# Optimization experiments

Measured on AMD Instinct MI355X. Metric: run time of the kernel, lower is better.

Reference implementation:

```python
import jax, jax.numpy as jnp
import numpy as np

EPS = 1e-8
NUM = 4


def rot_badmm(x, c1, c2, p0, q0, a0, a1, a2, a3, rho, mask, num=NUM, eps=EPS):
    """Entropic Bregman-ADMM regularized OT solver (badmm-e).
    x:(B,N,D) c1:(B,D,D) c2:(B,N,N) p0:(B,1,D) q0:(B,N,1) mask:(B,N,1)
    a0..a3, rho: (num,). Returns t:(B,N,D)."""
    lse = jax.nn.logsumexp
    log_t = jnp.log(q0 * p0 + eps)          # (B,N,D)
    log_s = log_t
    log_mu = jnp.log(p0)                    # (B,1,D)
    log_eta = jnp.log(q0 + eps)             # (B,N,1)
    log_p0 = jnp.log(p0)
    log_q0 = jnp.log(q0 + eps)
    z = jnp.zeros_like(log_t)
    z1 = jnp.zeros_like(p0)
    z2 = jnp.zeros_like(q0)
    for k in range(num):                    # fixed small unroll (num=4)
        n = min(k, a1.shape[0] - 1)
        tmp2 = jnp.matmul(jnp.matmul(c2, jnp.exp(log_s)), c1)   # (B,N,D)
        y = (x + a0[n] * tmp2 - z) / rho[n] + log_s
        log_t = (log_mu - lse(y, axis=2, keepdims=True)) + y    # row-normalize
        tmp2 = jnp.matmul(jnp.matmul(c2, jnp.exp(log_t)), c1)
        y = (z + a0[n] * tmp2 + rho[n] * log_t) / (a1[n] + rho[n])
        log_s = (log_eta - lse(y, axis=1, keepdims=True)) + y   # col-normalize
        t = jnp.exp(log_t) * mask
        s = jnp.exp(log_s) * mask
        z = z + rho[n] * (t - s)
        y = (rho[n] * log_mu + a2[n] * log_p0 - z1) / (rho[n] + a2[n])
        log_mu = y - lse(y, axis=2, keepdims=True)
        y = (rho[n] * log_eta + a3[n] * log_q0 - z2) / (rho[n] + a3[n])
        log_eta = y - lse(y, axis=1, keepdims=True)
        z1 = z1 + rho[n] * (jnp.exp(log_mu) - jnp.sum(t, axis=2, keepdims=True))
        z2 = z2 + rho[n] * (jnp.exp(log_eta) - jnp.sum(s, axis=1, keepdims=True))
    return jnp.exp(log_t) * mask


def setup_inputs() -> dict:
    key = jax.random.key(0)
    ks = jax.random.split(key, 10)
    B, N, D = 8, 1024, 512
    x = 0.1 * jax.random.normal(ks[0], (B, N, D), dtype=jnp.float32)
    c1 = 0.1 * jax.random.normal(ks[1], (B, D, D), dtype=jnp.float32)
    c2 = 0.1 * jax.random.normal(ks[2], (B, N, N), dtype=jnp.float32)
    p0 = jax.random.uniform(ks[3], (B, 1, D), dtype=jnp.float32) + 0.1
    p0 = p0 / jnp.sum(p0, axis=2, keepdims=True)        # valid marginal over D
    q0 = jax.random.uniform(ks[4], (B, N, 1), dtype=jnp.float32) + 0.1
    q0 = q0 / jnp.sum(q0, axis=1, keepdims=True)        # valid marginal over N
    a0 = jax.random.uniform(ks[5], (NUM,), dtype=jnp.float32) * 0.5 + 0.1
    a1 = jax.random.uniform(ks[6], (NUM,), dtype=jnp.float32) * 0.5 + 0.1
    a2 = jax.random.uniform(ks[7], (NUM,), dtype=jnp.float32) * 0.5 + 0.1
    a3 = jax.random.uniform(ks[8], (NUM,), dtype=jnp.float32) * 0.5 + 0.1
    rho = jax.random.uniform(ks[9], (NUM,), dtype=jnp.float32) * 0.5 + 0.5
    mask = jnp.ones((B, N, 1), dtype=jnp.float32)
    return {"x": x, "c1": c1, "c2": c2, "p0": p0, "q0": q0,
            "a0": a0, "a1": a1, "a2": a2, "a3": a3, "rho": rho,
            "mask": mask, "num": NUM}


def reference(x, c1, c2, p0, q0, a0, a1, a2, a3, rho, mask, num):
    return rot_badmm(x, c1, c2, p0, q0, a0, a1, a2, a3, rho, mask, num=num, eps=EPS)
```

## Files before the change

### kernel.cpp

```cpp
#include <hip/hip_runtime.h>
#include <math.h>

#define B_ 8
#define N_ 1024
#define D_ 512
#define CH 32
#define CHUNK (N_/CH)
#define EPSF 1e-8f

typedef unsigned short u16;
typedef __attribute__((ext_vector_type(8))) short bf16x8;
typedef __attribute__((ext_vector_type(4))) float f32x4;

static __device__ __forceinline__ u16 f2bf(float f){
  unsigned int u = __builtin_bit_cast(unsigned int, f);
  u = (u + 0x7FFFu + ((u >> 16) & 1u)) >> 16;
  return (u16)u;
}

static __device__ __forceinline__ float wredMax(float v){
#pragma unroll
  for (int o=32;o>=1;o>>=1) v = fmaxf(v, __shfl_xor(v,o,64));
  return v;
}
static __device__ __forceinline__ float wredSum(float v){
#pragma unroll
  for (int o=32;o>=1;o>>=1) v += __shfl_xor(v,o,64);
  return v;
}
static __device__ __forceinline__ float blockMax(float v, float* sm){
  v = wredMax(v);
  int w = threadIdx.x>>6, l = threadIdx.x&63;
  if (l==0) sm[w]=v;
  __syncthreads();
  float r = fmaxf(fmaxf(sm[0],sm[1]),fmaxf(sm[2],sm[3]));
  __syncthreads();
  return r;
}
static __device__ __forceinline__ float blockSum(float v, float* sm){
  v = wredSum(v);
  int w = threadIdx.x>>6, l = threadIdx.x&63;
  if (l==0) sm[w]=v;
  __syncthreads();
  float r = (sm[0]+sm[1])+(sm[2]+sm[3]);
  __syncthreads();
  return r;
}

__global__ __launch_bounds__(256)
void init_kernel(float* __restrict__ logS, float* __restrict__ Z,
                 const float* __restrict__ p0, const float* __restrict__ q0)
{
  long i = (long)blockIdx.x*256 + threadIdx.x;
  int d  = (int)(i & (D_-1));
  long bn = i >> 9;
  int b  = (int)(bn >> 10);
  logS[i] = logf(q0[bn]*p0[b*D_+d] + EPSF);
  Z[i] = 0.f;
}

__global__ __launch_bounds__(256)
void margInit_kernel(float* __restrict__ M, float* __restrict__ u,
                     float* __restrict__ Lv, float* __restrict__ p,
                     const float* __restrict__ p0, const float* __restrict__ q0)
{
  int b = blockIdx.x, t = threadIdx.x;
  for (int d = t; d < D_; d += 256){ M[b*D_+d] = logf(p0[b*D_+d]); u[b*D_+d] = 0.f; }
  for (int n = t; n < N_; n += 256){ Lv[b*N_+n] = logf(q0[b*N_+n] + EPSF); p[b*N_+n] = 0.f; }
}

__global__ __launch_bounds__(256)
void initEt_kernel(u16* __restrict__ Et, const float* __restrict__ p0,
                   const float* __restrict__ q0)
{
  long i = (long)blockIdx.x*256 + threadIdx.x;
  int n = (int)(i & (N_-1));
  long bd = i >> 10;
  int d = (int)(bd & (D_-1));
  int b = (int)(bd >> 9);
  Et[i] = f2bf(p0[b*D_+d]*q0[b*N_+n] + EPSF);
}

__global__ __launch_bounds__(256)
void conv_kernel(const float* __restrict__ src, u16* __restrict__ dst)
{
  long i = (long)blockIdx.x*256 + threadIdx.x;
  float4 v = ((const float4*)src)[i];
  ushort4 u;
  u.x=f2bf(v.x); u.y=f2bf(v.y); u.z=f2bf(v.z); u.w=f2bf(v.w);
  ((ushort4*)dst)[i] = u;
}

__global__ __launch_bounds__(256)
void tconv_kernel(const float* __restrict__ src, u16* __restrict__ dst, int R, int Ccols)
{
  __shared__ float tile[64][65];
  const int b = blockIdx.z;
  const long bb = (long)b*R*Ccols;
  const int r0 = blockIdx.x*64, c0 = blockIdx.y*64;
  const int c = threadIdx.x & 63, rr = threadIdx.x >> 6;
#pragma unroll
  for (int i=0;i<16;i++){
    int r = i*4 + rr;
    tile[r][c] = src[bb + (long)(r0+r)*Ccols + c0 + c];
  }
  __syncthreads();
#pragma unroll
  for (int i=0;i<16;i++){
    int r = i*4 + rr;
    dst[bb + (long)(c0+r)*R + r0 + c] = f2bf(tile[c][r]);
  }
}

template<int K, int OUT_BF16>
__global__ __launch_bounds__(256)
void gemm_mfma(const u16* __restrict__ Ab, const u16* __restrict__ Btb,
               void* __restrict__ Cp, long sA, long sB, long sC, int ldc)
{
  __shared__ __attribute__((aligned(16))) u16 As[128*72];
  __shared__ __attribute__((aligned(16))) u16 Bs[64*72];
  const int t = threadIdx.x;
  const int b = blockIdx.z;
  const int row0 = blockIdx.x*128, col0 = blockIdx.y*64;
  const int w = t>>6, l = t&63, lr = l&15, lg = l>>4;
  const int wm = w>>1, wn = w&1;

  f32x4 acc[4][2];
#pragma unroll
  for (int m=0;m<4;m++)
#pragma unroll
    for (int n=0;n<2;n++) acc[m][n] = (f32x4){0.f,0.f,0.f,0.f};

  const u16* Abb = Ab + (long)b*sA + (long)row0*K;
  const u16* Bbb = Btb + (long)b*sB + (long)col0*K;

  bf16x8 qa[4];
  bf16x8 qb[2];

#pragma unroll
  for (int i=0;i<4;i++){ int g=i*256+t; int r=g>>3, j=g&7;
    qa[i] = *(const bf16x8*)(Abb + (long)r*K + j*8); }
#pragma unroll
  for (int i=0;i<2;i++){ int g=i*256+t; int r=g>>3, j=g&7;
    qb[i] = *(const bf16x8*)(Bbb + (long)r*K + j*8); }

  for (int k0 = 0; k0 < K; k0 += 64) {
    __syncthreads();
#pragma unroll
    for (int i=0;i<4;i++){ int g=i*256+t; int r=g>>3, j=g&7;
      *(bf16x8*)&As[r*72 + j*8] = qa[i]; }
#pragma unroll
    for (int i=0;i<2;i++){ int g=i*256+t; int r=g>>3, j=g&7;
      *(bf16x8*)&Bs[r*72 + j*8] = qb[i]; }
    __syncthreads();
    if (k0 + 64 < K) {
      int kn = k0 + 64;
#pragma unroll
      for (int i=0;i<4;i++){ int g=i*256+t; int r=g>>3, j=g&7;
        qa[i] = *(const bf16x8*)(Abb + (long)r*K + kn + j*8); }
#pragma unroll
      for (int i=0;i<2;i++){ int g=i*256+t; int r=g>>3, j=g&7;
        qb[i] = *(const bf16x8*)(Bbb + (long)r*K + kn + j*8); }
    }
#pragma unroll
    for (int kk=0;kk<2;kk++){
      bf16x8 afr[4], bfr[2];
#pragma unroll
      for (int m=0;m<4;m++)
        afr[m] = *(const bf16x8*)&As[(wm*64 + m*16 + lr)*72 + kk*32 + lg*8];
#pragma unroll
      for (int n=0;n<2;n++)
        bfr[n] = *(const bf16x8*)&Bs[(wn*32 + n*16 + lr)*72 + kk*32 + lg*8];
#pragma unroll
      for (int m=0;m<4;m++)
#pragma unroll
        for (int n=0;n<2;n++)
          acc[m][n] = __builtin_amdgcn_mfma_f32_16x16x32_bf16(afr[m], bfr[n], acc[m][n], 0, 0, 0);
    }
  }

  if constexpr (OUT_BF16) {
    u16* C = (u16*)Cp + (long)b*sC;
#pragma unroll
    for (int m=0;m<4;m++)
#pragma unroll
      for (int n=0;n<2;n++){
        int grow = row0 + wm*64 + m*16 + lg*4;
        int gcol = col0 + wn*32 + n*16 + lr;
#pragma unroll
        for (int r4=0;r4<4;r4++)
          C[(long)(grow+r4)*ldc + gcol] = f2bf(acc[m][n][r4]);
      }
  } else {
    float* C = (float*)Cp + (long)b*sC;
#pragma unroll
    for (int m=0;m<4;m++)
#pragma unroll
      for (int n=0;n<2;n++){
        int grow = row0 + wm*64 + m*16 + lg*4;
        int gcol = col0 + wn*32 + n*16 + lr;
#pragma unroll
        for (int r4=0;r4<4;r4++)
          C[(long)(grow+r4)*ldc + gcol] = acc[m][n][r4];
      }
  }
}

__global__ __launch_bounds__(256)
void rowA_kernel(const float* __restrict__ x, const float* __restrict__ P2,
                 const float* __restrict__ Z, const float* __restrict__ logS,
                 const float* __restrict__ M, float* __restrict__ E,
                 const float* __restrict__ a0p, const float* __restrict__ rhop, int it)
{
  __shared__ float sm[4];
  const int bn = blockIdx.x;
  const int b = bn >> 10;
  const long base = (long)bn * D_;
  const float a0 = a0p[it], rho = rhop[it];
  const float inv_rho = 1.f/rho;
  const int d0 = threadIdx.x, d1 = d0 + 256;
  const long i0 = base + d0, i1 = base + d1;
  float y0 = (x[i0] + a0*P2[i0] - Z[i0])*inv_rho + logS[i0];
  float y1 = (x[i1] + a0*P2[i1] - Z[i1])*inv_rho + logS[i1];
  float Mx = blockMax(fmaxf(y0,y1), sm);
  float S = blockSum(expf(y0-Mx)+expf(y1-Mx), sm);
  float lse = Mx + logf(S);
  E[i0] = expf(M[b*D_+d0] - lse + y0);
  E[i1] = expf(M[b*D_+d1] - lse + y1);
}

__global__ __launch_bounds__(256)
void colS1_kernel(float* __restrict__ P2, const float* __restrict__ Z,
                  const float* __restrict__ E,
                  float* __restrict__ pMax, float* __restrict__ pSum,
                  const float* __restrict__ a0p, const float* __restrict__ a1p,
                  const float* __restrict__ rhop, int it)
{
  const int d = blockIdx.x*256 + threadIdx.x;
  const int ch = blockIdx.y, b = blockIdx.z;
  const float a0=a0p[it], rho=rhop[it];
  const float inv = 1.f/(a1p[it]+rho);
  long i = (long)b*N_*D_ + (long)(ch*CHUNK)*D_ + d;
  float m = -INFINITY, s = 0.f;
  for (int n=0;n<CHUNK;n++, i+=D_){
    float lt = logf(E[i] + 1e-37f);
    float yv = (Z[i] + a0*P2[i] + rho*lt)*inv;
    P2[i] = yv;
    float mn = fmaxf(m,yv);
    s = s*expf(m-mn) + expf(yv-mn);
    m = mn;
  }
  long pi = ((long)(b*D_+d))*CH + ch;
  pMax[pi]=m; pSum[pi]=s;
}

__global__ __launch_bounds__(256)
void colS2_kernel(const float* __restrict__ Yp, const float* __restrict__ E,
                  float* __restrict__ logS, float* __restrict__ Z,
                  const float* __restrict__ Lv,
                  const float* __restrict__ pMax, const float* __restrict__ pSum,
                  const float* __restrict__ maskp, u16* __restrict__ Et,
                  const float* __restrict__ rhop, int it)
{
  __shared__ u16 tile[CHUNK][258];
  const int tid = threadIdx.x;
  const int d0 = blockIdx.x*256;
  const int d = d0 + tid;
  const int ch = blockIdx.y, b = blockIdx.z;
  const int n0 = ch*CHUNK;
  const float rho = rhop[it];
  const long bd = (long)(b*D_+d);
  float M = -INFINITY;
#pragma unroll
  for (int c=0;c<CH;c++) M = fmaxf(M, pMax[bd*CH+c]);
  float S = 0.f;
#pragma unroll
  for (int c=0;c<CH;c++) S += pSum[bd*CH+c]*expf(pMax[bd*CH+c]-M);
  const float lseC = M + logf(S);
  long i = (long)b*N_*D_ + (long)n0*D_ + d;
  for (int n=0;n<CHUNK;n++, i+=D_){
    int gn = n0 + n;
    float msk = maskp[b*N_+gn];
    float ls = Lv[b*N_+gn] - lseC + Yp[i];
    logS[i] = ls;
    float es = expf(ls);
    tile[n][tid] = f2bf(es);
    Z[i] += rho*msk*(E[i] - es);
  }
  __syncthreads();
  const long EtBase = ((long)b*D_ + d0)*N_ + n0;
#pragma unroll
  for (int j=0;j<CHUNK;j++){
    int flat = j*256 + tid;
    int n_loc = flat & (CHUNK-1), d_loc = flat >> 5;
    Et[EtBase + (long)d_loc*N_ + n_loc] = tile[n_loc][d_loc];
  }
}

__global__ __launch_bounds__(256)
void margUpd_kernel(float* __restrict__ M, float* __restrict__ u,
                    float* __restrict__ Lv, float* __restrict__ p,
                    const float* __restrict__ p0, const float* __restrict__ q0,
                    const float* __restrict__ a2p, const float* __restrict__ a3p,
                    const float* __restrict__ rhop, int it)
{
  __shared__ float sm[4];
  const int b = blockIdx.x;
  const float rho = rhop[it];
  if (blockIdx.y == 0) {
    const float a2 = a2p[it], inv = 1.f/(rho+a2);
    const int d0 = threadIdx.x, d1 = d0+256;
    float A0 = (rho*M[b*D_+d0] + a2*logf(p0[b*D_+d0]) - u[b*D_+d0])*inv;
    float A1 = (rho*M[b*D_+d1] + a2*logf(p0[b*D_+d1]) - u[b*D_+d1])*inv;
    float Mx = blockMax(fmaxf(A0,A1), sm);
    float Sx = blockSum(expf(A0-Mx)+expf(A1-Mx), sm);
    float lse = Mx + logf(Sx);
    float M0 = A0 - lse, M1 = A1 - lse;
    M[b*D_+d0]=M0; M[b*D_+d1]=M1;
    u[b*D_+d0] += rho*expf(M0);
    u[b*D_+d1] += rho*expf(M1);
  } else {
    const float a3 = a3p[it], inv = 1.f/(rho+a3);
    const int n = threadIdx.x;
    float y0 = (rho*Lv[b*N_+n]     + a3*logf(q0[b*N_+n]+EPSF)     - p[b*N_+n])*inv;
    float y1 = (rho*Lv[b*N_+n+256] + a3*logf(q0[b*N_+n+256]+EPSF) - p[b*N_+n+256])*inv;
    float y2 = (rho*Lv[b*N_+n+512] + a3*logf(q0[b*N_+n+512]+EPSF) - p[b*N_+n+512])*inv;
    float y3 = (rho*Lv[b*N_+n+768] + a3*logf(q0[b*N_+n+768]+EPSF) - p[b*N_+n+768])*inv;
    float Mx = blockMax(fmaxf(fmaxf(y0,y1),fmaxf(y2,y3)), sm);
    float Sx = blockSum(expf(y0-Mx)+expf(y1-Mx)+expf(y2-Mx)+expf(y3-Mx), sm);
    float lse = Mx + logf(Sx);
    float L0=y0-lse, L1=y1-lse, L2=y2-lse, L3=y3-lse;
    Lv[b*N_+n]=L0; Lv[b*N_+n+256]=L1; Lv[b*N_+n+512]=L2; Lv[b*N_+n+768]=L3;
    p[b*N_+n]     += rho*expf(L0);
    p[b*N_+n+256] += rho*expf(L1);
    p[b*N_+n+512] += rho*expf(L2);
    p[b*N_+n+768] += rho*expf(L3);
  }
}

__global__ __launch_bounds__(256)
void final_kernel(float* __restrict__ E, const float* __restrict__ maskp)
{
  long i = (long)blockIdx.x*256 + threadIdx.x;
  long bn = i >> 9;
  E[i] = E[i]*maskp[bn];
}

extern "C" void kernel_launch(void* const* d_in, const int* in_sizes, int n_in,
                              void* d_out, int out_size, void* d_ws, size_t ws_size,
                              hipStream_t stream)
{
  const float* x    = (const float*)d_in[0];
  const float* c1   = (const float*)d_in[1];
  const float* c2   = (const float*)d_in[2];
  const float* p0   = (const float*)d_in[3];
  const float* q0   = (const float*)d_in[4];
  const float* a0   = (const float*)d_in[5];
  const float* a1   = (const float*)d_in[6];
  const float* a2   = (const float*)d_in[7];
  const float* a3   = (const float*)d_in[8];
  const float* rho  = (const float*)d_in[9];
  const float* mask = (const float*)d_in[10];

  const size_t BND = (size_t)B_*N_*D_;
  char* wb = (char*)d_ws;
  float* logS = (float*)(wb);
  float* Z    = logS + BND;
  float* P2   = Z    + BND;
  u16*  EtA = (u16*)(P2 + BND);
  u16*  T1b = EtA + BND;
  u16*  c1t = T1b + BND;
  u16*  c2b = c1t + (size_t)B_*D_*D_;
  float* pMax = (float*)(c2b + (size_t)B_*N_*N_);
  const size_t PART = (size_t)B_*D_*CH;
  float* pSum = pMax + PART;
  float* Mv   = pSum + PART;
  float* uv   = Mv + (size_t)B_*D_;
  float* Lv   = uv + (size_t)B_*D_;
  float* pv   = Lv + (size_t)B_*N_;
  float* E    = (float*)d_out;

  dim3 blk(256);
  const int gBND = (int)(BND/256);
  dim3 gT1(16, 8, B_);
  dim3 gTc(8, 8, B_);
  dim3 gG(8, 8, B_);
  dim3 gCol(D_/256, CH, B_);
  dim3 gMarg(B_, 2);

  const long sC2 = (long)N_*N_, sND = (long)N_*D_, sC1 = (long)D_*D_, sDN = (long)D_*N_;

  init_kernel<<<gBND, blk, 0, stream>>>(logS, Z, p0, q0);
  margInit_kernel<<<B_, blk, 0, stream>>>(Mv, uv, Lv, pv, p0, q0);
  initEt_kernel<<<gBND, blk, 0, stream>>>(EtA, p0, q0);
  tconv_kernel<<<gTc, blk, 0, stream>>>(c1, c1t, D_, D_);
  conv_kernel<<<(int)((size_t)B_*N_*N_/4/256), blk, 0, stream>>>(c2, c2b);

  for (int it=0; it<4; ++it) {
    gemm_mfma<1024,1><<<gG, blk, 0, stream>>>(c2b, EtA, T1b, sC2, sDN, sND, D_);
    gemm_mfma< 512,0><<<gG, blk, 0, stream>>>(T1b, c1t, P2, sND, sC1, sND, D_);
    rowA_kernel<<<B_*N_, blk, 0, stream>>>(x, P2, Z, logS, Mv, E, a0, rho, it);
    tconv_kernel<<<gT1, blk, 0, stream>>>(E, EtA, N_, D_);
    gemm_mfma<1024,1><<<gG, blk, 0, stream>>>(c2b, EtA, T1b, sC2, sDN, sND, D_);
    gemm_mfma< 512,0><<<gG, blk, 0, stream>>>(T1b, c1t, P2, sND, sC1, sND, D_);
    colS1_kernel<<<gCol, blk, 0, stream>>>(P2, Z, E, pMax, pSum, a0, a1, rho, it);
    colS2_kernel<<<gCol, blk, 0, stream>>>(P2, E, logS, Z, Lv, pMax, pSum, mask, EtA, rho, it);
    margUpd_kernel<<<gMarg, blk, 0, stream>>>(Mv, uv, Lv, pv, p0, q0, a2, a3, rho, it);
  }
  final_kernel<<<gBND, blk, 0, stream>>>(E, mask);
}
```

Measured before the change: 599.7 us.

## Reassociate chained matmul, drop transposes, double-buffer LDS in MFMA GEMM

The product c2·X·c1 is now computed as c2·(X·c1). The first GEMM writes its output transposed as bf16, so X can stay in natural row-major layout. This removes the tconv transpose kernel after rowA and the LDS transpose at the end of colS2, which now write bf16 X directly. The GEMM also gains double-buffered LDS with explicit barriers so global loads overlap MFMA compute. The tradeoff is more LDS per block and strided transposed stores in the epilogue.

```diff
diff --git a/kernel.cpp b/kernel.cpp
--- a/kernel.cpp
+++ b/kernel.cpp
@@ -17,6 +17,12 @@
   u = (u + 0x7FFFu + ((u >> 16) & 1u)) >> 16;
   return (u16)u;
 }
+
+#define BARSYNC() do { \
+  asm volatile("s_waitcnt lgkmcnt(0)" ::: "memory"); \
+  __builtin_amdgcn_s_barrier(); \
+  __builtin_amdgcn_sched_barrier(0); \
+} while(0)
 
 static __device__ __forceinline__ float wredMax(float v){
 #pragma unroll
@@ -70,15 +76,14 @@
 }
 
 __global__ __launch_bounds__(256)
-void initEt_kernel(u16* __restrict__ Et, const float* __restrict__ p0,
-                   const float* __restrict__ q0)
+void initX_kernel(u16* __restrict__ Xb, const float* __restrict__ p0,
+                  const float* __restrict__ q0)
 {
   long i = (long)blockIdx.x*256 + threadIdx.x;
-  int n = (int)(i & (N_-1));
-  long bd = i >> 10;
-  int d = (int)(bd & (D_-1));
-  int b = (int)(bd >> 9);
-  Et[i] = f2bf(p0[b*D_+d]*q0[b*N_+n] + EPSF);
+  int d = (int)(i & (D_-1));
+  long bn = i >> 9;
+  int b = (int)(bn >> 10);
+  Xb[i] = f2bf(p0[b*D_+d]*q0[bn] + EPSF);
 }
 
 __global__ __launch_bounds__(256)
@@ -112,13 +117,13 @@
   }
 }
 
-template<int K, int OUT_BF16>
+template<int K, int OUT_TRANS>
 __global__ __launch_bounds__(256)
 void gemm_mfma(const u16* __restrict__ Ab, const u16* __restrict__ Btb,
                void* __restrict__ Cp, long sA, long sB, long sC, int ldc)
 {
-  __shared__ __attribute__((aligned(16))) u16 As[128*72];
-  __shared__ __attribute__((aligned(16))) u16 Bs[64*72];
+  __shared__ __attribute__((aligned(16))) u16 As[2][128*72];
+  __shared__ __attribute__((aligned(16))) u16 Bs[2][64*72];
   const int t = threadIdx.x;
   const int b = blockIdx.z;
   const int row0 = blockIdx.x*128, col0 = blockIdx.y*64;
@@ -134,52 +139,60 @@
   const u16* Abb = Ab + (long)b*sA + (long)row0*K;
   const u16* Bbb = Btb + (long)b*sB + (long)col0*K;
 
-  bf16x8 qa[4];
-  bf16x8 qb[2];
-
-#pragma unroll
-  for (int i=0;i<4;i++){ int g=i*256+t; int r=g>>3, j=g&7;
-    qa[i] = *(const bf16x8*)(Abb + (long)r*K + j*8); }
-#pragma unroll
-  for (int i=0;i<2;i++){ int g=i*256+t; int r=g>>3, j=g&7;
-    qb[i] = *(const bf16x8*)(Bbb + (long)r*K + j*8); }
-
-  for (int k0 = 0; k0 < K; k0 += 64) {
-    __syncthreads();
+  bf16x8 a0r[4], b0r[2], a1r[4], b1r[2];
+
+  auto loadA = [&](bf16x8* q, int kk0){
 #pragma unroll
     for (int i=0;i<4;i++){ int g=i*256+t; int r=g>>3, j=g&7;
-      *(bf16x8*)&As[r*72 + j*8] = qa[i]; }
+      q[i] = *(const bf16x8*)(Abb + (long)r*K + kk0 + j*8); }
+  };
+  auto loadB = [&](bf16x8* q, int kk0){
 #pragma unroll
     for (int i=0;i<2;i++){ int g=i*256+t; int r=g>>3, j=g&7;
-      *(bf16x8*)&Bs[r*72 + j*8] = qb[i]; }
-    __syncthreads();
-    if (k0 + 64 < K) {
-      int kn = k0 + 64;
-#pragma unroll
-      for (int i=0;i<4;i++){ int g=i*256+t; int r=g>>3, j=g&7;
-        qa[i] = *(const bf16x8*)(Abb + (long)r*K + kn + j*8); }
-#pragma unroll
-      for (int i=0;i<2;i++){ int g=i*256+t; int r=g>>3, j=g&7;
-        qb[i] = *(const bf16x8*)(Bbb + (long)r*K + kn + j*8); }
-    }
+      q[i] = *(const bf16x8*)(Bbb + (long)r*K + kk0 + j*8); }
+  };
+  auto writeLDS = [&](int buf, const bf16x8* qa, const bf16x8* qb){
+#pragma unroll
+    for (int i=0;i<4;i++){ int g=i*256+t; int r=g>>3, j=g&7;
+      *(bf16x8*)&As[buf][r*72 + j*8] = qa[i]; }
+#pragma unroll
+    for (int i=0;i<2;i++){ int g=i*256+t; int r=g>>3, j=g&7;
+      *(bf16x8*)&Bs[buf][r*72 + j*8] = qb[i]; }
+  };
+  auto compute = [&](int buf){
 #pragma unroll
     for (int kk=0;kk<2;kk++){
       bf16x8 afr[4], bfr[2];
 #pragma unroll
       for (int m=0;m<4;m++)
-        afr[m] = *(const bf16x8*)&As[(wm*64 + m*16 + lr)*72 + kk*32 + lg*8];
+        afr[m] = *(const bf16x8*)&As[buf][(wm*64 + m*16 + lr)*72 + kk*32 + lg*8];
 #pragma unroll
       for (int n=0;n<2;n++)
-        bfr[n] = *(const bf16x8*)&Bs[(wn*32 + n*16 + lr)*72 + kk*32 + lg*8];
+        bfr[n] = *(const bf16x8*)&Bs[buf][(wn*32 + n*16 + lr)*72 + kk*32 + lg*8];
 #pragma unroll
       for (int m=0;m<4;m++)
 #pragma unroll
         for (int n=0;n<2;n++)
           acc[m][n] = __builtin_amdgcn_mfma_f32_16x16x32_bf16(afr[m], bfr[n], acc[m][n], 0, 0, 0);
     }
-  }
-
-  if constexpr (OUT_BF16) {
+  };
+
+  loadA(a0r, 0); loadB(b0r, 0);
+  loadA(a1r, 64); loadB(b1r, 64);
+  writeLDS(0, a0r, b0r);
+
+  for (int k0 = 0; k0 < K; k0 += 128) {
+    BARSYNC();
+    if (k0+128 < K){ loadA(a0r, k0+128); loadB(b0r, k0+128); }
+    compute(0);
+    writeLDS(1, a1r, b1r);
+    BARSYNC();
+    if (k0+192 < K){ loadA(a1r, k0+192); loadB(b1r, k0+192); }
+    compute(1);
+    if (k0+128 < K) writeLDS(0, a0r, b0r);
+  }
+
+  if constexpr (OUT_TRANS) {
     u16* C = (u16*)Cp + (long)b*sC;
 #pragma unroll
     for (int m=0;m<4;m++)
@@ -187,9 +200,10 @@
       for (int n=0;n<2;n++){
         int grow = row0 + wm*64 + m*16 + lg*4;
         int gcol = col0 + wn*32 + n*16 + lr;
-#pragma unroll
-        for (int r4=0;r4<4;r4++)
-          C[(long)(grow+r4)*ldc + gcol] = f2bf(acc[m][n][r4]);
+        ushort4 v;
+        v.x=f2bf(acc[m][n][0]); v.y=f2bf(acc[m][n][1]);
+        v.z=f2bf(acc[m][n][2]); v.w=f2bf(acc[m][n][3]);
+        *(ushort4*)&C[(long)gcol*ldc + grow] = v;
       }
   } else {
     float* C = (float*)Cp + (long)b*sC;
@@ -210,6 +224,7 @@
 void rowA_kernel(const float* __restrict__ x, const float* __restrict__ P2,
                  const float* __restrict__ Z, const float* __restrict__ logS,
                  const float* __restrict__ M, float* __restrict__ E,
+                 u16* __restrict__ Xb,
                  const float* __restrict__ a0p, const float* __restrict__ rhop, int it)
 {
   __shared__ float sm[4];
@@ -225,8 +240,10 @@
   float Mx = blockMax(fmaxf(y0,y1), sm);
   float S = blockSum(expf(y0-Mx)+expf(y1-Mx), sm);
   float lse = Mx + logf(S);
-  E[i0] = expf(M[b*D_+d0] - lse + y0);
-  E[i1] = expf(M[b*D_+d1] - lse + y1);
+  float e0 = expf(M[b*D_+d0] - lse + y0);
+  float e1 = expf(M[b*D_+d1] - lse + y1);
+  E[i0] = e0; E[i1] = e1;
+  Xb[i0] = f2bf(e0); Xb[i1] = f2bf(e1);
 }
 
 __global__ __launch_bounds__(256)
@@ -259,13 +276,11 @@
                   float* __restrict__ logS, float* __restrict__ Z,
                   const float* __restrict__ Lv,
                   const float* __restrict__ pMax, const float* __restrict__ pSum,
-                  const float* __restrict__ maskp, u16* __restrict__ Et,
+                  const float* __restrict__ maskp, u16* __restrict__ Xb,
                   const float* __restrict__ rhop, int it)
 {
-  __shared__ u16 tile[CHUNK][258];
   const int tid = threadIdx.x;
-  const int d0 = blockIdx.x*256;
-  const int d = d0 + tid;
+  const int d = blockIdx.x*256 + tid;
   const int ch = blockIdx.y, b = blockIdx.z;
   const int n0 = ch*CHUNK;
   const float rho = rhop[it];
@@ -284,16 +299,8 @@
     float ls = Lv[b*N_+gn] - lseC + Yp[i];
     logS[i] = ls;
     float es = expf(ls);
-    tile[n][tid] = f2bf(es);
+    Xb[i] = f2bf(es);
     Z[i] += rho*msk*(E[i] - es);
-  }
-  __syncthreads();
-  const long EtBase = ((long)b*D_ + d0)*N_ + n0;
-#pragma unroll
-  for (int j=0;j<CHUNK;j++){
-    int flat = j*256 + tid;
-    int n_loc = flat & (CHUNK-1), d_loc = flat >> 5;
-    Et[EtBase + (long)d_loc*N_ + n_loc] = tile[n_loc][d_loc];
   }
 }
 
@@ -367,9 +374,9 @@
   float* logS = (float*)(wb);
   float* Z    = logS + BND;
   float* P2   = Z    + BND;
-  u16*  EtA = (u16*)(P2 + BND);
-  u16*  T1b = EtA + BND;
-  u16*  c1t = T1b + BND;
+  u16*  Xb  = (u16*)(P2 + BND);
+  u16*  Yt  = Xb + BND;
+  u16*  c1t = Yt + BND;
   u16*  c2b = c1t + (size_t)B_*D_*D_;
   float* pMax = (float*)(c2b + (size_t)B_*N_*N_);
   const size_t PART = (size_t)B_*D_*CH;
@@ -382,7 +389,6 @@
 
   dim3 blk(256);
   const int gBND = (int)(BND/256);
-  dim3 gT1(16, 8, B_);
   dim3 gTc(8, 8, B_);
   dim3 gG(8, 8, B_);
   dim3 gCol(D_/256, CH, B_);
@@ -392,19 +398,18 @@
 
   init_kernel<<<gBND, blk, 0, stream>>>(logS, Z, p0, q0);
   margInit_kernel<<<B_, blk, 0, stream>>>(Mv, uv, Lv, pv, p0, q0);
-  initEt_kernel<<<gBND, blk, 0, stream>>>(EtA, p0, q0);
+  initX_kernel<<<gBND, blk, 0, stream>>>(Xb, p0, q0);
   tconv_kernel<<<gTc, blk, 0, stream>>>(c1, c1t, D_, D_);
   conv_kernel<<<(int)((size_t)B_*N_*N_/4/256), blk, 0, stream>>>(c2, c2b);
 
   for (int it=0; it<4; ++it) {
-    gemm_mfma<1024,1><<<gG, blk, 0, stream>>>(c2b, EtA, T1b, sC2, sDN, sND, D_);
-    gemm_mfma< 512,0><<<gG, blk, 0, stream>>>(T1b, c1t, P2, sND, sC1, sND, D_);
-    rowA_kernel<<<B_*N_, blk, 0, stream>>>(x, P2, Z, logS, Mv, E, a0, rho, it);
-    tconv_kernel<<<gT1, blk, 0, stream>>>(E, EtA, N_, D_);
-    gemm_mfma<1024,1><<<gG, blk, 0, stream>>>(c2b, EtA, T1b, sC2, sDN, sND, D_);
-    gemm_mfma< 512,0><<<gG, blk, 0, stream>>>(T1b, c1t, P2, sND, sC1, sND, D_);
+    gemm_mfma< 512,1><<<gG, blk, 0, stream>>>(Xb, c1t, Yt, sND, sC1, sDN, N_);
+    gemm_mfma<1024,0><<<gG, blk, 0, stream>>>(c2b, Yt, P2, sC2, sDN, sND, D_);
+    rowA_kernel<<<B_*N_, blk, 0, stream>>>(x, P2, Z, logS, Mv, E, Xb, a0, rho, it);
+    gemm_mfma< 512,1><<<gG, blk, 0, stream>>>(Xb, c1t, Yt, sND, sC1, sDN, N_);
+    gemm_mfma<1024,0><<<gG, blk, 0, stream>>>(c2b, Yt, P2, sC2, sDN, sND, D_);
     colS1_kernel<<<gCol, blk, 0, stream>>>(P2, Z, E, pMax, pSum, a0, a1, rho, it);
-    colS2_kernel<<<gCol, blk, 0, stream>>>(P2, E, logS, Z, Lv, pMax, pSum, mask, EtA, rho, it);
+    colS2_kernel<<<gCol, blk, 0, stream>>>(P2, E, logS, Z, Lv, pMax, pSum, mask, Xb, rho, it);
     margUpd_kernel<<<gMarg, blk, 0, stream>>>(Mv, uv, Lv, pv, p0, q0, a2, a3, rho, it);
   }
   final_kernel<<<gBND, blk, 0, stream>>>(E, mask);
```

Measured after the change: 584.2 us. 2.6% less time.
